# Performance work log

Measured on AMD Instinct MI355X. Metric: run time of the kernel, lower is better.

Reference implementation:

```python
import jax, jax.numpy as jnp
import numpy as np

B, T, C = 2, 2048, 1024
NH, NKV, HD, NG = 16, 8, 64, 8   # heads, kv heads, head_dim, global heads
NG_KV = NG * NKV // NH           # global kv heads = 4
VE_CH = 32                       # ve_gate input channels
WIN = 1024                       # local sliding-window (left) size


def setup_inputs() -> dict:
    key = jax.random.key(0)
    ks = jax.random.split(key, 8)
    x = jax.random.normal(ks[0], (B, T, C), jnp.float32)
    ve = jax.random.normal(ks[1], (B, T, NKV * HD), jnp.float32)
    # true rotary tables over half the head dim
    half = HD // 2
    inv_freq = 1.0 / (10000.0 ** (np.arange(half, dtype=np.float64) / half))
    ang = np.arange(T, dtype=np.float64)[:, None] * inv_freq[None, :]
    cos = jnp.asarray(np.cos(ang), jnp.float32)[None, :, None, :]  # [1,T,1,32]
    sin = jnp.asarray(np.sin(ang), jnp.float32)[None, :, None, :]
    s = C ** -0.5
    Wq = jax.random.normal(ks[2], (C, NH * HD), jnp.float32) * s
    Wk = jax.random.normal(ks[3], (C, NKV * HD), jnp.float32) * s
    Wv = jax.random.normal(ks[4], (C, NKV * HD), jnp.float32) * s
    Wproj = jax.random.normal(ks[5], (C, C), jnp.float32) * s
    Wg = jax.random.normal(ks[6], (VE_CH, NKV), jnp.float32) * (VE_CH ** -0.5)
    return dict(x=x, ve=ve, cos=cos, sin=sin, Wq=Wq, Wk=Wk, Wv=Wv,
                Wproj=Wproj, Wg=Wg, window=WIN)


def _rope(x, cos, sin):
    d = x.shape[-1] // 2
    x1, x2 = x[..., :d], x[..., d:]
    return jnp.concatenate([x1 * cos + x2 * sin, -x1 * sin + x2 * cos], axis=-1)


def _rms_norm(x):
    eps = jnp.asarray(jnp.finfo(x.dtype).eps, x.dtype)
    return x * jax.lax.rsqrt(jnp.mean(x * x, axis=-1, keepdims=True) + eps)


def _gqa_attn(q, k, v, left_window):
    # q: [B,T,Hq,D]; k,v: [B,T,Hk,D]; GQA with g = Hq//Hk queries per kv head.
    b, t, hq, d = q.shape
    hk = k.shape[2]
    g = hq // hk
    qg = q.reshape(b, t, hk, g, d)
    scores = jnp.einsum('bqhgd,bkhd->bhgqk', qg, k) * (d ** -0.5)
    i = jnp.arange(t)[:, None]
    j = jnp.arange(t)[None, :]
    if left_window < 0:
        mask = j <= i                       # full causal
    else:
        mask = (j <= i) & ((i - j) <= left_window)  # causal sliding window
    scores = jnp.where(mask, scores, jnp.asarray(-1e30, scores.dtype))
    p = jax.nn.softmax(scores, axis=-1)
    out = jnp.einsum('bhgqk,bkhd->bqhgd', p, v)
    return out.reshape(b, t, hq, d)


def reference(x, ve, cos, sin, Wq, Wk, Wv, Wproj, Wg, window):
    b, t, c = x.shape
    q = (x @ Wq).reshape(b, t, NH, HD)
    k = (x @ Wk).reshape(b, t, NKV, HD)
    v = (x @ Wv).reshape(b, t, NKV, HD)
    # value-embedding gating: gate = 2*sigmoid(Linear(x[..., :32])) per kv head
    gate = 2.0 * jax.nn.sigmoid(x[..., :VE_CH] @ Wg)       # [B,T,NKV]
    v = v + gate[..., None] * ve.reshape(b, t, NKV, HD)
    # inline RoPE then RMSNorm on q and k
    q = _rms_norm(_rope(q, cos, sin))
    k = _rms_norm(_rope(k, cos, sin))
    # split global (full causal) vs local (windowed) head groups
    y_global = _gqa_attn(q[:, :, :NG], k[:, :, :NG_KV], v[:, :, :NG_KV], -1)
    y_local = _gqa_attn(q[:, :, NG:], k[:, :, NG_KV:], v[:, :, NG_KV:], window)
    y = jnp.concatenate([y_global, y_local], axis=2).reshape(b, t, c)
    return y @ Wproj
```

## Files before the change

### kernel.cpp

```cpp
#include <hip/hip_runtime.h>
#include <hip/hip_bf16.h>
#include <math.h>

typedef __bf16 bf16x8 __attribute__((ext_vector_type(8)));
typedef __bf16 bf16x4 __attribute__((ext_vector_type(4)));
typedef float  f32x4  __attribute__((ext_vector_type(4)));

#define MFMA16(a, b, c) __builtin_amdgcn_mfma_f32_16x16x32_bf16((a), (b), (c), 0, 0, 0)

__device__ __forceinline__ void gload16(const void* g, void* lds) {
    __builtin_amdgcn_global_load_lds(
        (const __attribute__((address_space(1))) uint32_t*)g,
        (__attribute__((address_space(3))) uint32_t*)lds, 16, 0, 0);
}

__global__ __launch_bounds__(256)
void prep2_kernel(const float* __restrict__ x, __bf16* __restrict__ xb,
                  const float* __restrict__ Wq, const float* __restrict__ Wk,
                  const float* __restrict__ Wv, const float* __restrict__ Wproj,
                  __bf16* __restrict__ wqkvt, __bf16* __restrict__ wprojt) {
    const int bx = blockIdx.x;
    const int tid = threadIdx.x;
    if (bx < 4096) {
        int i = bx * 256 + tid;
        float4 v = reinterpret_cast<const float4*>(x)[i];
        bf16x4 o = { (__bf16)v.x, (__bf16)v.y, (__bf16)v.z, (__bf16)v.w };
        *reinterpret_cast<bf16x4*>(xb + (size_t)i * 4) = o;
        return;
    }
    __shared__ __bf16 Ts[64 * 72];
    const int idx = bx - 4096;
    const int z = idx >> 8;
    const float* W = (z == 0) ? Wq : (z == 1) ? Wk : (z == 2) ? Wv : Wproj;
    __bf16* dst = (z == 3) ? wprojt : wqkvt;
    const int N = (z == 1 || z == 2) ? 512 : 1024;
    const int nt_off = (z == 1) ? 1024 : (z == 2) ? 1536 : 0;
    const int n0 = (idx & 15) * 64, k0 = ((idx >> 4) & 15) * 64;
    if (n0 >= N) return;
    {
        int r = tid >> 2;
        int c0 = (tid & 3) * 16;
        const float4* s4 = reinterpret_cast<const float4*>(
            W + (size_t)(k0 + r) * N + n0 + c0);
        float val[16];
        #pragma unroll
        for (int q = 0; q < 4; ++q) {
            float4 v = s4[q];
            val[q * 4 + 0] = v.x; val[q * 4 + 1] = v.y;
            val[q * 4 + 2] = v.z; val[q * 4 + 3] = v.w;
        }
        #pragma unroll
        for (int j = 0; j < 16; ++j) Ts[(c0 + j) * 72 + r] = (__bf16)val[j];
    }
    __syncthreads();
    {
        int n = tid >> 2, kg = (tid & 3) * 16;
        __bf16* out = dst + (size_t)(nt_off + n0 + n) * 1024 + k0 + kg;
        bf16x8 t0 = *reinterpret_cast<const bf16x8*>(&Ts[n * 72 + kg]);
        bf16x8 t1 = *reinterpret_cast<const bf16x8*>(&Ts[n * 72 + kg + 8]);
        *reinterpret_cast<bf16x8*>(out) = t0;
        *reinterpret_cast<bf16x8*>(out + 8) = t1;
    }
}

template <typename OutT>
__global__ __launch_bounds__(256)
void gemm_bf16(const __bf16* __restrict__ A, const __bf16* __restrict__ Bt,
               OutT* __restrict__ C, int M, int N, int K) {
    __shared__ __align__(16) __bf16 As[128 * 64];
    __shared__ __align__(16) __bf16 Bs[128 * 64];
    const int tid = threadIdx.x;
    const int lane = tid & 63, w = tid >> 6;
    const int wr = w >> 1, wc = w & 1;
    const int nwg = gridDim.x * gridDim.y;
    const int id = blockIdx.y * gridDim.x + blockIdx.x;
    const int nid = (id & 7) * (nwg >> 3) + (id >> 3);
    const int bxs = nid % gridDim.x, bys = nid / gridDim.x;
    const int bm = bys * 128, bn = bxs * 128;
    const int lhi = lane >> 4, llo = lane & 15;
    const int gsrc = (lane & 7) ^ ((lane >> 3) & 7);

    f32x4 acc[4][4] = {};

    for (int k0 = 0; k0 < K; k0 += 64) {
        __syncthreads();
        const __bf16* Ab = A + (size_t)bm * K + k0;
        const __bf16* Bb = Bt + (size_t)bn * K + k0;
        #pragma unroll
        for (int rr = 0; rr < 4; ++rr) {
            int c = rr * 4 + w;
            int r = c * 8 + (lane >> 3);
            gload16(Ab + (size_t)r * K + gsrc * 8, (char*)As + c * 1024);
            gload16(Bb + (size_t)r * K + gsrc * 8, (char*)Bs + c * 1024);
        }
        __syncthreads();

        #pragma unroll
        for (int ks = 0; ks < 2; ++ks) {
            bf16x8 af[4], bfr[4];
            int g = ks * 4 + lhi;
            #pragma unroll
            for (int i = 0; i < 4; ++i) {
                int ra = wr * 64 + i * 16 + llo;
                af[i] = *reinterpret_cast<const bf16x8*>(
                    (const char*)As + ra * 128 + ((g ^ (ra & 7)) << 4));
                int rb = wc * 64 + i * 16 + llo;
                bfr[i] = *reinterpret_cast<const bf16x8*>(
                    (const char*)Bs + rb * 128 + ((g ^ (rb & 7)) << 4));
            }
            #pragma unroll
            for (int i = 0; i < 4; ++i)
                #pragma unroll
                for (int j = 0; j < 4; ++j)
                    acc[i][j] = MFMA16(af[i], bfr[j], acc[i][j]);
        }
    }

    #pragma unroll
    for (int i = 0; i < 4; ++i) {
        #pragma unroll
        for (int j = 0; j < 4; ++j) {
            int col = bn + wc * 64 + j * 16 + llo;
            #pragma unroll
            for (int r = 0; r < 4; ++r) {
                int row = bm + wr * 64 + i * 16 + lhi * 4 + r;
                C[(size_t)row * N + col] = (OutT)acc[i][j][r];
            }
        }
    }
}

__global__ __launch_bounds__(256)
void post_kernel(__bf16* __restrict__ qkv, const float* __restrict__ x,
                 const float* __restrict__ ve, const float* __restrict__ Wg,
                 const float* __restrict__ cosb, const float* __restrict__ sinb,
                 __bf16* __restrict__ vT) {
    const int id = blockIdx.x;
    const int tid = threadIdx.x;
    if (id < 24576) {
        const int u = id >> 10;
        const int row = (id & 1023) * 4 + (tid >> 6);
        const int d = tid & 63;
        const int t = row & 2047;
        const int off = (u < 16) ? u * 64 : 1024 + (u - 16) * 64;
        __bf16* p = qkv + (size_t)row * 2048 + off;
        float v = (float)p[d];
        float partner = __shfl(v, d ^ 32, 64);
        float r;
        if (d < 32) {
            float cs = cosb[t * 32 + d], sn = sinb[t * 32 + d];
            r = v * cs + partner * sn;
        } else {
            float cs = cosb[t * 32 + d - 32], sn = sinb[t * 32 + d - 32];
            r = -partner * sn + v * cs;
        }
        float s = r * r;
        #pragma unroll
        for (int mm = 1; mm < 64; mm <<= 1) s += __shfl_xor(s, mm, 64);
        r *= rsqrtf(s * (1.0f / 64.0f) + 1.1920929e-07f);
        if (u < 16) r *= 0.18033688011116012f;
        p[d] = (__bf16)r;
    } else {
        __shared__ __bf16 Ts[64 * 72];
        const int rem = id - 24576;
        const int ch = rem & 63;
        const int h = rem >> 6;
        {
            int r = tid >> 2, c0 = (tid & 3) * 16;
            int grow = ch * 64 + r;
            float gz = 0.f;
            {
                const float* xr = x + (size_t)grow * 1024 + (tid & 3) * 8;
                #pragma unroll
                for (int i = 0; i < 8; ++i)
                    gz = fmaf(xr[i], Wg[((tid & 3) * 8 + i) * 8 + h], gz);
                gz += __shfl_xor(gz, 1, 64);
                gz += __shfl_xor(gz, 2, 64);
            }
            float g = 2.0f / (1.0f + expf(-gz));
            const __bf16* vp = qkv + (size_t)grow * 2048 + 1536 + h * 64 + c0;
            const float* vep = ve + (size_t)grow * 512 + h * 64 + c0;
            bf16x8 v0 = *reinterpret_cast<const bf16x8*>(vp);
            bf16x8 v1 = *reinterpret_cast<const bf16x8*>(vp + 8);
            #pragma unroll
            for (int j = 0; j < 8; ++j) {
                Ts[(c0 + j) * 72 + r]     = (__bf16)((float)v0[j] + g * vep[j]);
                Ts[(c0 + 8 + j) * 72 + r] = (__bf16)((float)v1[j] + g * vep[8 + j]);
            }
        }
        __syncthreads();
        {
            int d = tid >> 2, t0l = (tid & 3) * 16;
            int b = ch >> 5, tloc = (ch & 31) * 64;
            __bf16* out = vT + ((size_t)((b * 8 + h) * 64 + d)) * 2048 + tloc + t0l;
            bf16x8 t0 = *reinterpret_cast<const bf16x8*>(&Ts[d * 72 + t0l]);
            bf16x8 t1 = *reinterpret_cast<const bf16x8*>(&Ts[d * 72 + t0l + 8]);
            *reinterpret_cast<bf16x8*>(out) = t0;
            *reinterpret_cast<bf16x8*>(out + 8) = t1;
        }
    }
}

__global__ __launch_bounds__(256, 6)
void attn_mfma(const __bf16* __restrict__ qkv, const __bf16* __restrict__ vT,
               __bf16* __restrict__ y, const int* __restrict__ winp) {
    __shared__ __align__(16) __bf16 Ks[64 * 64];
    __shared__ __align__(16) __bf16 VTs[64 * 64];
    __shared__ __align__(16) __bf16 Ps[4][16 * 64];

    const int bid = blockIdx.x;
    const int kvh = bid & 7;
    int tdec = bid >> 3;
    const int b = tdec & 1; tdec >>= 1;
    const int qh = tdec & 1;
    const int qt = 31 - (tdec >> 1);
    const int h = (kvh < 4) ? (kvh * 2 + qh) : (8 + (kvh - 4) * 2 + qh);
    const int q0 = qt * 64;
    const int tid = threadIdx.x, lane = tid & 63, w = tid >> 6;
    const int lhi = lane >> 4, llo = lane & 15;
    const int gsrc = (lane & 7) ^ ((lane >> 3) & 7);
    const int win = (h < 8) ? -1 : winp[0];
    const int winv = (win < 0) ? (1 << 30) : win;

    const __bf16* kbase = qkv + (size_t)(b * 2048) * 2048 + 1024 + kvh * 64;
    const __bf16* vtbase = vT + ((size_t)((b * 8 + kvh) * 64)) * 2048;

    int kts = 0;
    if (win >= 0) { int s = q0 - win; if (s > 0) kts = s >> 6; }

    const __bf16* qrow = qkv + (size_t)(b * 2048 + q0 + w * 16 + llo) * 2048
                         + h * 64 + lhi * 8;
    bf16x8 qf[2];
    qf[0] = *(const bf16x8*)(qrow);
    qf[1] = *(const bf16x8*)(qrow + 32);

    auto STAGE = [&](int ktx) {
        #pragma unroll
        for (int rr = 0; rr < 2; ++rr) {
            int c = rr * 4 + w;
            int r = c * 8 + (lane >> 3);
            gload16(kbase + (size_t)(ktx * 64 + r) * 2048 + gsrc * 8,
                    (char*)Ks + c * 1024);
            gload16(vtbase + (size_t)r * 2048 + ktx * 64 + gsrc * 8,
                    (char*)VTs + c * 1024);
        }
    };

    f32x4 oaccT[4] = {};
    float lrow = 0.f;

    const int pswz = (llo & 7) << 4;

    for (int kt = kts; kt <= qt; ++kt) {
        STAGE(kt);
        __syncthreads();

        f32x4 sacc[4] = {};
        __builtin_amdgcn_s_setprio(1);
        #pragma unroll
        for (int ks = 0; ks < 2; ++ks) {
            #pragma unroll
            for (int kj = 0; kj < 4; ++kj) {
                int rb = kj * 16 + llo;
                bf16x8 bk = *(const bf16x8*)((const char*)&Ks[0]
                    + rb * 128 + (((ks * 4 + lhi) ^ (rb & 7)) << 4));
                sacc[kj] = MFMA16(bk, qf[ks], sacc[kj]);
            }
        }
        __builtin_amdgcn_s_setprio(0);

        const bool needMask = (kt == qt) || (win >= 0 && kt * 64 < q0 + 63 - winv);

        float sv[16];
        #pragma unroll
        for (int kj = 0; kj < 4; ++kj)
            #pragma unroll
            for (int r = 0; r < 4; ++r)
                sv[kj * 4 + r] = sacc[kj][r];
        if (needMask) {
            int qrowi = q0 + w * 16 + llo;
            #pragma unroll
            for (int kj = 0; kj < 4; ++kj)
                #pragma unroll
                for (int r = 0; r < 4; ++r) {
                    int key = kt * 64 + kj * 16 + lhi * 4 + r;
                    bool ok = (key <= qrowi) && (qrowi - key <= winv);
                    if (!ok) sv[kj * 4 + r] = -__builtin_inff();
                }
        }

        float p[16];
        #pragma unroll
        for (int t = 0; t < 16; ++t)
            p[t] = __builtin_amdgcn_exp2f(sv[t]);

        #pragma unroll
        for (int kj = 0; kj < 4; ++kj) {
            bf16x4 pk = { (__bf16)p[kj * 4 + 0], (__bf16)p[kj * 4 + 1],
                          (__bf16)p[kj * 4 + 2], (__bf16)p[kj * 4 + 3] };
            *(bf16x4*)((char*)&Ps[w][0]
                + ((llo * 128 + kj * 32 + lhi * 8) ^ pswz)) = pk;
        }

        #pragma unroll
        for (int st = 8; st >= 1; st >>= 1)
            #pragma unroll
            for (int t = 0; t < st; ++t) p[t] += p[t + st];
        lrow += p[0];

        __builtin_amdgcn_s_setprio(1);
        #pragma unroll
        for (int ks = 0; ks < 2; ++ks) {
            bf16x8 ap = *(const bf16x8*)((const char*)&Ps[w][0]
                + ((llo * 128 + ks * 64 + lhi * 16) ^ pswz));
            #pragma unroll
            for (int dj = 0; dj < 4; ++dj) {
                int rv = dj * 16 + llo;
                bf16x8 bv = *(const bf16x8*)((const char*)&VTs[0]
                    + rv * 128 + (((ks * 4 + lhi) ^ (rv & 7)) << 4));
                oaccT[dj] = MFMA16(bv, ap, oaccT[dj]);
            }
        }
        __builtin_amdgcn_s_setprio(0);

        __syncthreads();
    }

    lrow += __shfl_xor(lrow, 16, 64);
    lrow += __shfl_xor(lrow, 32, 64);

    float inv = 1.0f / lrow;
    int row = b * 2048 + q0 + w * 16 + llo;
    #pragma unroll
    for (int dj = 0; dj < 4; ++dj) {
        bf16x4 o = { (__bf16)(oaccT[dj][0] * inv), (__bf16)(oaccT[dj][1] * inv),
                     (__bf16)(oaccT[dj][2] * inv), (__bf16)(oaccT[dj][3] * inv) };
        *(bf16x4*)(&y[(size_t)row * 1024 + h * 64 + dj * 16 + lhi * 4]) = o;
    }
}

extern "C" void kernel_launch(void* const* d_in, const int* in_sizes, int n_in,
                              void* d_out, int out_size, void* d_ws, size_t ws_size,
                              hipStream_t stream) {
    const float* x     = (const float*)d_in[0];
    const float* ve    = (const float*)d_in[1];
    const float* cosb  = (const float*)d_in[2];
    const float* sinb  = (const float*)d_in[3];
    const float* Wq    = (const float*)d_in[4];
    const float* Wk    = (const float*)d_in[5];
    const float* Wv    = (const float*)d_in[6];
    const float* Wproj = (const float*)d_in[7];
    const float* Wg    = (const float*)d_in[8];
    const int*   winp  = (const int*)d_in[9];

    char* ws = (char*)d_ws;
    __bf16* qkv    = (__bf16*)(ws);
    __bf16* vT     = (__bf16*)(ws + (16u << 20));
    __bf16* ybuf   = (__bf16*)(ws + (20u << 20));
    __bf16* xb     = (__bf16*)(ws + (28u << 20));
    __bf16* wqkvt  = (__bf16*)(ws + (36u << 20));
    __bf16* wprojt = (__bf16*)(ws + (40u << 20));

    prep2_kernel<<<5120, 256, 0, stream>>>(x, xb, Wq, Wk, Wv, Wproj, wqkvt, wprojt);
    gemm_bf16<__bf16><<<dim3(16, 32), 256, 0, stream>>>(xb, wqkvt, qkv, 4096, 2048, 1024);
    post_kernel<<<25088, 256, 0, stream>>>(qkv, x, ve, Wg, cosb, sinb, vT);
    attn_mfma<<<1024, 256, 0, stream>>>(qkv, vT, ybuf, winp);
    gemm_bf16<float><<<dim3(8, 32), 256, 0, stream>>>(ybuf, wprojt, (float*)d_out, 4096, 1024, 1024);
}
```

Measured before the change: 117.4 us.

## Split attention key range into chunks with separate combine kernel

Attention work is split along the key dimension into chunks of up to 8 key tiles (split-K / flash-decoding style). Each block writes unnormalized partial outputs in bf16 plus row sums, and a new combine kernel sums the partials and normalizes. The aim is to balance the causal triangle across more blocks and shorten the longest blocks. The cost is an extra launch, extra memory traffic for the partials, and bf16 rounding of partial sums. Blocks whose chunk holds no unmasked key tiles exit early. Because softmax uses no running max, summing the partials needs no rescaling.

```diff
diff --git a/kernel.cpp b/kernel.cpp
--- a/kernel.cpp
+++ b/kernel.cpp
@@ -203,17 +203,24 @@
 
 __global__ __launch_bounds__(256, 6)
 void attn_mfma(const __bf16* __restrict__ qkv, const __bf16* __restrict__ vT,
-               __bf16* __restrict__ y, const int* __restrict__ winp) {
+               __bf16* __restrict__ Opart, float* __restrict__ lpart,
+               const int* __restrict__ winp) {
     __shared__ __align__(16) __bf16 Ks[64 * 64];
     __shared__ __align__(16) __bf16 VTs[64 * 64];
     __shared__ __align__(16) __bf16 Ps[4][16 * 64];
 
     const int bid = blockIdx.x;
     const int kvh = bid & 7;
-    int tdec = bid >> 3;
-    const int b = tdec & 1; tdec >>= 1;
-    const int qh = tdec & 1;
-    const int qt = 31 - (tdec >> 1);
+    const int t = bid >> 3;
+    const int b = (t >> 1) & 1;
+    const int qh = t & 1;
+    const int pp = t >> 2;
+    const int p = 79 - pp;
+    int qt, c;
+    if (p < 8)       { qt = p;                 c = 0; }
+    else if (p < 24) { qt = 8 + ((p - 8) >> 1);  c = (p - 8) & 1; }
+    else if (p < 48) { qt = 16 + (p - 24) / 3;   c = (p - 24) % 3; }
+    else             { qt = 24 + ((p - 48) >> 2); c = (p - 48) & 3; }
     const int h = (kvh < 4) ? (kvh * 2 + qh) : (8 + (kvh - 4) * 2 + qh);
     const int q0 = qt * 64;
     const int tid = threadIdx.x, lane = tid & 63, w = tid >> 6;
@@ -222,11 +229,14 @@
     const int win = (h < 8) ? -1 : winp[0];
     const int winv = (win < 0) ? (1 << 30) : win;
 
+    int kts = 0;
+    if (win >= 0) { int s = q0 - win; if (s > 0) kts = s >> 6; }
+    const int tstart = (kts > c * 8) ? kts : c * 8;
+    const int tend = (qt < c * 8 + 7) ? qt : c * 8 + 7;
+    if (tstart > tend) return;
+
     const __bf16* kbase = qkv + (size_t)(b * 2048) * 2048 + 1024 + kvh * 64;
     const __bf16* vtbase = vT + ((size_t)((b * 8 + kvh) * 64)) * 2048;
-
-    int kts = 0;
-    if (win >= 0) { int s = q0 - win; if (s > 0) kts = s >> 6; }
 
     const __bf16* qrow = qkv + (size_t)(b * 2048 + q0 + w * 16 + llo) * 2048
                          + h * 64 + lhi * 8;
@@ -237,12 +247,12 @@
     auto STAGE = [&](int ktx) {
         #pragma unroll
         for (int rr = 0; rr < 2; ++rr) {
-            int c = rr * 4 + w;
-            int r = c * 8 + (lane >> 3);
+            int cc = rr * 4 + w;
+            int r = cc * 8 + (lane >> 3);
             gload16(kbase + (size_t)(ktx * 64 + r) * 2048 + gsrc * 8,
-                    (char*)Ks + c * 1024);
+                    (char*)Ks + cc * 1024);
             gload16(vtbase + (size_t)r * 2048 + ktx * 64 + gsrc * 8,
-                    (char*)VTs + c * 1024);
+                    (char*)VTs + cc * 1024);
         }
     };
 
@@ -251,7 +261,7 @@
 
     const int pswz = (llo & 7) << 4;
 
-    for (int kt = kts; kt <= qt; ++kt) {
+    for (int kt = tstart; kt <= tend; ++kt) {
         STAGE(kt);
         __syncthreads();
 
@@ -289,15 +299,15 @@
                 }
         }
 
-        float p[16];
-        #pragma unroll
-        for (int t = 0; t < 16; ++t)
-            p[t] = __builtin_amdgcn_exp2f(sv[t]);
+        float pe[16];
+        #pragma unroll
+        for (int tt = 0; tt < 16; ++tt)
+            pe[tt] = __builtin_amdgcn_exp2f(sv[tt]);
 
         #pragma unroll
         for (int kj = 0; kj < 4; ++kj) {
-            bf16x4 pk = { (__bf16)p[kj * 4 + 0], (__bf16)p[kj * 4 + 1],
-                          (__bf16)p[kj * 4 + 2], (__bf16)p[kj * 4 + 3] };
+            bf16x4 pk = { (__bf16)pe[kj * 4 + 0], (__bf16)pe[kj * 4 + 1],
+                          (__bf16)pe[kj * 4 + 2], (__bf16)pe[kj * 4 + 3] };
             *(bf16x4*)((char*)&Ps[w][0]
                 + ((llo * 128 + kj * 32 + lhi * 8) ^ pswz)) = pk;
         }
@@ -305,8 +315,8 @@
         #pragma unroll
         for (int st = 8; st >= 1; st >>= 1)
             #pragma unroll
-            for (int t = 0; t < st; ++t) p[t] += p[t + st];
-        lrow += p[0];
+            for (int tt = 0; tt < st; ++tt) pe[tt] += pe[tt + st];
+        lrow += pe[0];
 
         __builtin_amdgcn_s_setprio(1);
         #pragma unroll
@@ -329,14 +339,61 @@
     lrow += __shfl_xor(lrow, 16, 64);
     lrow += __shfl_xor(lrow, 32, 64);
 
-    float inv = 1.0f / lrow;
-    int row = b * 2048 + q0 + w * 16 + llo;
+    const size_t slot = ((size_t)((b * 16 + h) * 32 + qt)) * 4 + c;
+    __bf16* op = Opart + slot * 4096;
+    const int r64 = w * 16 + llo;
     #pragma unroll
     for (int dj = 0; dj < 4; ++dj) {
-        bf16x4 o = { (__bf16)(oaccT[dj][0] * inv), (__bf16)(oaccT[dj][1] * inv),
-                     (__bf16)(oaccT[dj][2] * inv), (__bf16)(oaccT[dj][3] * inv) };
-        *(bf16x4*)(&y[(size_t)row * 1024 + h * 64 + dj * 16 + lhi * 4]) = o;
-    }
+        bf16x4 o = { (__bf16)oaccT[dj][0], (__bf16)oaccT[dj][1],
+                     (__bf16)oaccT[dj][2], (__bf16)oaccT[dj][3] };
+        *(bf16x4*)(op + r64 * 64 + dj * 16 + lhi * 4) = o;
+    }
+    if (lhi == 0) lpart[slot * 64 + r64] = lrow;
+}
+
+__global__ __launch_bounds__(256)
+void combine_kernel(const __bf16* __restrict__ Opart,
+                    const float* __restrict__ lpart,
+                    __bf16* __restrict__ ybuf, const int* __restrict__ winp) {
+    const int bid = blockIdx.x;
+    const int qt = bid & 31, h = (bid >> 5) & 15, b = bid >> 9;
+    const int q0 = qt * 64;
+    int cmin = 0;
+    if (h >= 8) {
+        int s = q0 - winp[0];
+        int kts = (s > 0) ? (s >> 6) : 0;
+        cmin = kts >> 3;
+    }
+    const int cmax = qt >> 3;
+    const int tid = threadIdx.x;
+    const int r64 = tid >> 2;
+    const int cg = (tid & 3) << 4;
+    const size_t slotbase = ((size_t)((b * 16 + h) * 32 + qt)) * 4;
+    float acc[16];
+    #pragma unroll
+    for (int j = 0; j < 16; ++j) acc[j] = 0.f;
+    float lsum = 0.f;
+    for (int c = cmin; c <= cmax; ++c) {
+        const __bf16* op = Opart + (slotbase + c) * 4096 + r64 * 64 + cg;
+        bf16x8 a0 = *(const bf16x8*)op;
+        bf16x8 a1 = *(const bf16x8*)(op + 8);
+        #pragma unroll
+        for (int j = 0; j < 8; ++j) {
+            acc[j] += (float)a0[j];
+            acc[8 + j] += (float)a1[j];
+        }
+        lsum += lpart[(slotbase + c) * 64 + r64];
+    }
+    float inv = 1.0f / lsum;
+    __bf16* yp = ybuf + (size_t)(b * 2048 + q0 + r64) * 1024 + h * 64 + cg;
+    bf16x8 o0, o1;
+    #pragma unroll
+    for (int j = 0; j < 8; ++j) {
+        o0[j] = (__bf16)(acc[j] * inv);
+        o1[j] = (__bf16)(acc[8 + j] * inv);
+    }
+    *(bf16x8*)yp = o0;
+    *(bf16x8*)(yp + 8) = o1;
 }
 
 extern "C" void kernel_launch(void* const* d_in, const int* in_sizes, int n_in,
@@ -360,10 +417,13 @@
     __bf16* xb     = (__bf16*)(ws + (28u << 20));
     __bf16* wqkvt  = (__bf16*)(ws + (36u << 20));
     __bf16* wprojt = (__bf16*)(ws + (40u << 20));
+    __bf16* Opart  = (__bf16*)(ws + (64u << 20));
+    float*  lpart  = (float*) (ws + (96u << 20));
 
     prep2_kernel<<<5120, 256, 0, stream>>>(x, xb, Wq, Wk, Wv, Wproj, wqkvt, wprojt);
     gemm_bf16<__bf16><<<dim3(16, 32), 256, 0, stream>>>(xb, wqkvt, qkv, 4096, 2048, 1024);
     post_kernel<<<25088, 256, 0, stream>>>(qkv, x, ve, Wg, cosb, sinb, vT);
-    attn_mfma<<<1024, 256, 0, stream>>>(qkv, vT, ybuf, winp);
+    attn_mfma<<<2560, 256, 0, stream>>>(qkv, vT, Opart, lpart, winp);
+    combine_kernel<<<1024, 256, 0, stream>>>(Opart, lpart, ybuf, winp);
     gemm_bf16<float><<<dim3(8, 32), 256, 0, stream>>>(ybuf, wprojt, (float*)d_out, 4096, 1024, 1024);
 }
```

Result: slower. 120.8 us (+2.9%).
